# Kernel tuning notes

Measured on AMD Instinct MI355X. Metric: run time of the kernel, lower is better.

## Reference

```python
import jax, jax.numpy as jnp
import numpy as np

N = 4096
NFEAT = 512
NHID = 64
NHEADS = 8
NCLASS = 41
ALPHA = 0.2          # LeakyReLU negative slope
NEG = -9e15          # mask fill value from the torch code
EDGE_P = 0.004       # ~16 avg degree


def _xavier_uniform(key, shape, gain=1.414):
    fan_in, fan_out = shape[-2], shape[-1]
    limit = gain * np.sqrt(6.0 / (fan_in + fan_out))
    return jax.random.uniform(key, shape, jnp.float32, -limit, limit)


def setup_inputs() -> dict:
    key = jax.random.key(0)
    ks = jax.random.split(key, 6)
    x = jax.random.normal(ks[0], (N, NFEAT), jnp.float32)
    # sparse random graph, densified (module calls adj.to_dense()); add self-loops
    adj = (jax.random.uniform(ks[1], (N, N)) < EDGE_P).astype(jnp.float32)
    adj = jnp.maximum(adj, jnp.eye(N, dtype=jnp.float32))
    # 8 attention heads (nfeat -> nhid), stacked
    W_heads = _xavier_uniform(ks[2], (NHEADS, NFEAT, NHID))
    a_heads = _xavier_uniform(ks[3], (NHEADS, 2 * NHID, 1))
    # output attention layer (nhid*nheads -> nclass)
    W_out = _xavier_uniform(ks[4], (NHEADS * NHID, NCLASS))
    a_out = _xavier_uniform(ks[5], (2 * NCLASS, 1))
    return {"x": x, "adj": adj, "W_heads": W_heads, "a_heads": a_heads,
            "W_out": W_out, "a_out": a_out}


def _leaky_relu(e):
    return jnp.where(e > 0, e, ALPHA * e)


def reference(x, adj, W_heads, a_heads, W_out, a_out):
    # inference mode: all dropout layers are identity (training=False)
    mask = adj > 0                                   # [N, N]
    # ---- multi-head GAT layer (concat=True, ELU inside layer) ----
    Wh = jnp.einsum('nf,hfd->hnd', x, W_heads)       # [H, N, D]
    a1 = a_heads[:, :NHID, 0]                        # [H, D]
    a2 = a_heads[:, NHID:, 0]                        # [H, D]
    s1 = jnp.einsum('hnd,hd->hn', Wh, a1)            # [H, N]
    s2 = jnp.einsum('hnd,hd->hn', Wh, a2)            # [H, N]
    e = _leaky_relu(s1[:, :, None] + s2[:, None, :])  # [H, N, N]
    att = jax.nn.softmax(jnp.where(mask[None], e, NEG), axis=-1)
    h = jax.nn.elu(jnp.einsum('hnm,hmd->hnd', att, Wh))   # [H, N, D]
    h = jnp.transpose(h, (1, 0, 2)).reshape(N, NHEADS * NHID)  # concat heads
    # ---- output GAT layer (concat=False) + ELU (with_relu=True) ----
    Wh2 = h @ W_out                                  # [N, C]
    e2 = _leaky_relu(Wh2 @ a_out[:NCLASS] + (Wh2 @ a_out[NCLASS:]).T)  # [N, N]
    att2 = jax.nn.softmax(jnp.where(mask, e2, NEG), axis=-1)
    out = jax.nn.elu(att2 @ Wh2)                     # [N, C]
    # mode='t', multi_label falsy -> log_softmax
    return jax.nn.log_softmax(out, axis=1)
```

## Files before the change

### kernel.cpp

```cpp
#include <hip/hip_runtime.h>
#include <hip/hip_bf16.h>
#include <math.h>


#define N 4096
#define NFEAT 512
#define NHID 64
#define NHEADS 8
#define NCLASS 41
#define NCPAD 48
#define ALPHA 0.2f
#define ELLW 64

using short8  = __attribute__((ext_vector_type(8))) short;
using floatx4 = __attribute__((ext_vector_type(4))) float;

__device__ __forceinline__ float wred_max(float v) {
#pragma unroll
  for (int o = 32; o; o >>= 1) v = fmaxf(v, __shfl_xor(v, o, 64));
  return v;
}
__device__ __forceinline__ float wred_sum(float v) {
#pragma unroll
  for (int o = 32; o; o >>= 1) v += __shfl_xor(v, o, 64);
  return v;
}

__device__ __forceinline__ void split_bf16(float v, short& hi, short& lo) {
  __hip_bfloat16 hb = __float2bfloat16(v);
  float hf = __bfloat162float(hb);
  __hip_bfloat16 lb = __float2bfloat16(v - hf);
  hi = *reinterpret_cast<short*>(&hb);
  lo = *reinterpret_cast<short*>(&lb);
}

__global__ __launch_bounds__(256) void setup(const float* __restrict__ x,
                                             const float* __restrict__ W,
                                             const float* __restrict__ W_out,
                                             const float* __restrict__ adj,
                                             short* __restrict__ Xhi,
                                             short* __restrict__ Xlo,
                                             short* __restrict__ Wthi,
                                             short* __restrict__ Wtlo,
                                             short* __restrict__ WOhi,
                                             short* __restrict__ WOlo,
                                             int* __restrict__ cols,
                                             int* __restrict__ cnts) {
  if (blockIdx.x >= 3168) {
    __shared__ int c;
    const int row = blockIdx.x - 3168;
    if (threadIdx.x == 0) c = 0;
    __syncthreads();
    const float4* arow = (const float4*)(adj + (size_t)row * N);
    for (int j4 = threadIdx.x; j4 < N / 4; j4 += 256) {
      float4 v = arow[j4];
      if (v.x > 0.f) { int p = atomicAdd(&c, 1); if (p < ELLW) cols[row * ELLW + p] = j4 * 4 + 0; }
      if (v.y > 0.f) { int p = atomicAdd(&c, 1); if (p < ELLW) cols[row * ELLW + p] = j4 * 4 + 1; }
      if (v.z > 0.f) { int p = atomicAdd(&c, 1); if (p < ELLW) cols[row * ELLW + p] = j4 * 4 + 2; }
      if (v.w > 0.f) { int p = atomicAdd(&c, 1); if (p < ELLW) cols[row * ELLW + p] = j4 * 4 + 3; }
    }
    __syncthreads();
    if (threadIdx.x == 0) cnts[row] = min(c, ELLW);
  } else if (blockIdx.x < 2048) {
    const int t = blockIdx.x * 256 + threadIdx.x;
    const float4 v = ((const float4*)x)[t];
    short h0, l0, h1, l1, h2, l2, h3, l3;
    split_bf16(v.x, h0, l0);
    split_bf16(v.y, h1, l1);
    split_bf16(v.z, h2, l2);
    split_bf16(v.w, h3, l3);
    ((short4*)Xhi)[t] = make_short4(h0, h1, h2, h3);
    ((short4*)Xlo)[t] = make_short4(l0, l1, l2, l3);
  } else if (blockIdx.x < 3072) {
    const int t = (blockIdx.x - 2048) * 256 + threadIdx.x;
    const int h = t >> 15, r = t & 32767;
    const int d = r >> 9, k = r & 511;
    float v = W[(size_t)h * 32768 + (size_t)k * 64 + d];
    short hi, lo;
    split_bf16(v, hi, lo);
    Wthi[(size_t)h * 32768 + d * 512 + k] = hi;
    Wtlo[(size_t)h * 32768 + d * 512 + k] = lo;
  } else {
    const int t = (blockIdx.x - 3072) * 256 + threadIdx.x;
    const int c = t >> 9, k = t & 511;
    float v = (c < NCLASS) ? W_out[(size_t)k * NCLASS + c] : 0.f;
    short hi, lo;
    split_bf16(v, hi, lo);
    WOhi[c * 512 + k] = hi;
    WOlo[c * 512 + k] = lo;
  }
}

__global__ __launch_bounds__(256) void wh_gemm_mfma(
    const short* __restrict__ Xhi, const short* __restrict__ Xlo,
    const short* __restrict__ Wthi, const short* __restrict__ Wtlo,
    const float* __restrict__ a_heads,
    float* __restrict__ Wh, float* __restrict__ s1, float* __restrict__ s2) {
  __shared__ __align__(16) short Ahi[64 * 72];
  __shared__ __align__(16) short Alo[64 * 72];
  __shared__ __align__(16) short Bhi[64 * 72];
  __shared__ __align__(16) short Blo[64 * 72];
  const int id = blockIdx.x;
  const int h = (id >> 3) & 7;
  const int tile = (id & 7) + ((id >> 6) << 3);
  const int n0 = tile * 64;
  const int tid = threadIdx.x;
  const int w = tid >> 6, L = tid & 63;

  floatx4 acc[4];
#pragma unroll
  for (int f = 0; f < 4; f++) acc[f] = (floatx4){0.f, 0.f, 0.f, 0.f};

  for (int k0 = 0; k0 < NFEAT; k0 += 64) {
    __syncthreads();
#pragma unroll
    for (int i = 0; i < 2; i++) {
      const int g = tid + 256 * i;
      const int row = g >> 3, kg = (g & 7) * 8;
      const size_t asrc = (size_t)(n0 + row) * NFEAT + k0 + kg;
      *(uint4*)&Ahi[row * 72 + kg] = *(const uint4*)&Xhi[asrc];
      *(uint4*)&Alo[row * 72 + kg] = *(const uint4*)&Xlo[asrc];
      const size_t bsrc = (size_t)h * 32768 + (size_t)row * 512 + k0 + kg;
      *(uint4*)&Bhi[row * 72 + kg] = *(const uint4*)&Wthi[bsrc];
      *(uint4*)&Blo[row * 72 + kg] = *(const uint4*)&Wtlo[bsrc];
    }
    __syncthreads();
#pragma unroll
    for (int ks = 0; ks < 2; ks++) {
      const int koff = ks * 32 + (L >> 4) * 8;
      short8 ahi = *(const short8*)&Ahi[(w * 16 + (L & 15)) * 72 + koff];
      short8 alo = *(const short8*)&Alo[(w * 16 + (L & 15)) * 72 + koff];
#pragma unroll
      for (int f = 0; f < 4; f++) {
        short8 bhi = *(const short8*)&Bhi[(f * 16 + (L & 15)) * 72 + koff];
        short8 blo = *(const short8*)&Blo[(f * 16 + (L & 15)) * 72 + koff];
        acc[f] = __builtin_amdgcn_mfma_f32_16x16x32_bf16(ahi, bhi, acc[f], 0, 0, 0);
        acc[f] = __builtin_amdgcn_mfma_f32_16x16x32_bf16(ahi, blo, acc[f], 0, 0, 0);
        acc[f] = __builtin_amdgcn_mfma_f32_16x16x32_bf16(alo, bhi, acc[f], 0, 0, 0);
      }
    }
  }

  const int q = L >> 4, c16 = L & 15;
  float a1v[4], a2v[4];
#pragma unroll
  for (int f = 0; f < 4; f++) {
    a1v[f] = a_heads[h * 128 + f * 16 + c16];
    a2v[f] = a_heads[h * 128 + 64 + f * 16 + c16];
  }
  float p1[4] = {0.f, 0.f, 0.f, 0.f}, p2[4] = {0.f, 0.f, 0.f, 0.f};
#pragma unroll
  for (int f = 0; f < 4; f++)
#pragma unroll
    for (int r = 0; r < 4; r++) {
      const float vv = acc[f][r];
      const int row = n0 + w * 16 + q * 4 + r;
      Wh[((size_t)(h << 12) + row) * NHID + f * 16 + c16] = vv;
      p1[r] += vv * a1v[f];
      p2[r] += vv * a2v[f];
    }
#pragma unroll
  for (int r = 0; r < 4; r++)
#pragma unroll
    for (int o = 1; o < 16; o <<= 1) {
      p1[r] += __shfl_xor(p1[r], o, 64);
      p2[r] += __shfl_xor(p2[r], o, 64);
    }
  if (c16 == 0) {
    const int row = n0 + w * 16 + q * 4;
#pragma unroll
    for (int r = 0; r < 4; r++) {
      s1[(h << 12) + row + r] = p1[r];
      s2[(h << 12) + row + r] = p2[r];
    }
  }
}

__global__ __launch_bounds__(256) void att1_kernel(
    const float* __restrict__ Wh, const float* __restrict__ s1,
    const float* __restrict__ s2, const int* __restrict__ cols,
    const int* __restrict__ cnts, short* __restrict__ Hhi,
    short* __restrict__ Hlo) {
  __shared__ float pj[4][68];
  __shared__ int jj[4][68];
  const int w = threadIdx.x >> 6, lane = threadIdx.x & 63;
  const int pair = blockIdx.x * 4 + w;
  const int h = pair >> 12, i = pair & (N - 1);
  const int cnt = cnts[i];
  const float s1i = s1[(h << 12) + i];
  const float* s2h = s2 + (h << 12);
  float e0 = -1e30f;
  int j0 = 0;
  if (lane < cnt) {
    j0 = cols[i * ELLW + lane];
    float t = s1i + s2h[j0];
    e0 = t > 0.f ? t : ALPHA * t;
  }
  const float m = wred_max(e0);
  float p = (lane < cnt) ? expf(e0 - m) : 0.f;
  const float S = wred_sum(p);
  p *= 1.f / S;
  pj[w][lane] = p;
  jj[w][lane] = (lane < cnt) ? j0 : 0;
  if (lane < 4) { pj[w][64 + lane] = 0.f; jj[w][64 + lane] = 0; }
  __syncthreads();
  const int grp = lane >> 4, c4 = lane & 15;
  const float* Whh = Wh + (((size_t)h << 12)) * NHID;
  float4 acc = make_float4(0.f, 0.f, 0.f, 0.f);
  for (int t0 = 0; t0 < cnt; t0 += 4) {
    const float pt = pj[w][t0 + grp];
    const int jt = jj[w][t0 + grp];
    const float4 v = *(const float4*)&Whh[(size_t)jt * NHID + c4 * 4];
    acc.x += pt * v.x; acc.y += pt * v.y; acc.z += pt * v.z; acc.w += pt * v.w;
  }
#pragma unroll
  for (int off = 16; off <= 32; off <<= 1) {
    acc.x += __shfl_xor(acc.x, off, 64);
    acc.y += __shfl_xor(acc.y, off, 64);
    acc.z += __shfl_xor(acc.z, off, 64);
    acc.w += __shfl_xor(acc.w, off, 64);
  }
  if (grp == 0) {
    const float o0 = acc.x > 0.f ? acc.x : expf(acc.x) - 1.f;
    const float o1 = acc.y > 0.f ? acc.y : expf(acc.y) - 1.f;
    const float o2 = acc.z > 0.f ? acc.z : expf(acc.z) - 1.f;
    const float o3 = acc.w > 0.f ? acc.w : expf(acc.w) - 1.f;
    short h0, l0, h1, l1, h2, l2, h3, l3;
    split_bf16(o0, h0, l0);
    split_bf16(o1, h1, l1);
    split_bf16(o2, h2, l2);
    split_bf16(o3, h3, l3);
    const size_t base = (size_t)i * 512 + h * 64 + c4 * 4;
    *(short4*)&Hhi[base] = make_short4(h0, h1, h2, h3);
    *(short4*)&Hlo[base] = make_short4(l0, l1, l2, l3);
  }
}

__global__ __launch_bounds__(256) void gemm2_mfma(
    const short* __restrict__ Hhi, const short* __restrict__ Hlo,
    const short* __restrict__ WOhi, const short* __restrict__ WOlo,
    const float* __restrict__ a_out,
    float* __restrict__ Wh2, float* __restrict__ s1b, float* __restrict__ s2b) {
  __shared__ __align__(16) short Ahi[64 * 72];
  __shared__ __align__(16) short Alo[64 * 72];
  __shared__ __align__(16) short Bhi[NCPAD * 72];
  __shared__ __align__(16) short Blo[NCPAD * 72];
  const int n0 = blockIdx.x * 64;
  const int tid = threadIdx.x;
  const int w = tid >> 6, L = tid & 63;

  floatx4 acc[3];
#pragma unroll
  for (int f = 0; f < 3; f++) acc[f] = (floatx4){0.f, 0.f, 0.f, 0.f};

  for (int k0 = 0; k0 < 512; k0 += 64) {
    __syncthreads();
#pragma unroll
    for (int i = 0; i < 2; i++) {
      const int g = tid + 256 * i;
      const int row = g >> 3, kg = (g & 7) * 8;
      const size_t asrc = (size_t)(n0 + row) * 512 + k0 + kg;
      *(uint4*)&Ahi[row * 72 + kg] = *(const uint4*)&Hhi[asrc];
      *(uint4*)&Alo[row * 72 + kg] = *(const uint4*)&Hlo[asrc];
      if (g < NCPAD * 8) {
        const size_t bsrc = (size_t)row * 512 + k0 + kg;
        *(uint4*)&Bhi[row * 72 + kg] = *(const uint4*)&WOhi[bsrc];
        *(uint4*)&Blo[row * 72 + kg] = *(const uint4*)&WOlo[bsrc];
      }
    }
    __syncthreads();
#pragma unroll
    for (int ks = 0; ks < 2; ks++) {
      const int koff = ks * 32 + (L >> 4) * 8;
      short8 ahi = *(const short8*)&Ahi[(w * 16 + (L & 15)) * 72 + koff];
      short8 alo = *(const short8*)&Alo[(w * 16 + (L & 15)) * 72 + koff];
#pragma unroll
      for (int f = 0; f < 3; f++) {
        short8 bhi = *(const short8*)&Bhi[(f * 16 + (L & 15)) * 72 + koff];
        short8 blo = *(const short8*)&Blo[(f * 16 + (L & 15)) * 72 + koff];
        acc[f] = __builtin_amdgcn_mfma_f32_16x16x32_bf16(ahi, bhi, acc[f], 0, 0, 0);
        acc[f] = __builtin_amdgcn_mfma_f32_16x16x32_bf16(ahi, blo, acc[f], 0, 0, 0);
        acc[f] = __builtin_amdgcn_mfma_f32_16x16x32_bf16(alo, bhi, acc[f], 0, 0, 0);
      }
    }
  }

  const int q = L >> 4, c16 = L & 15;
  float a1v[3], a2v[3];
#pragma unroll
  for (int f = 0; f < 3; f++) {
    const int col = f * 16 + c16;
    a1v[f] = (col < NCLASS) ? a_out[col] : 0.f;
    a2v[f] = (col < NCLASS) ? a_out[NCLASS + col] : 0.f;
  }
  float p1[4] = {0.f, 0.f, 0.f, 0.f}, p2[4] = {0.f, 0.f, 0.f, 0.f};
#pragma unroll
  for (int f = 0; f < 3; f++)
#pragma unroll
    for (int r = 0; r < 4; r++) {
      const float vv = acc[f][r];
      const int col = f * 16 + c16;
      const int row = n0 + w * 16 + q * 4 + r;
      if (col < NCLASS) Wh2[(size_t)row * NCLASS + col] = vv;
      p1[r] += vv * a1v[f];
      p2[r] += vv * a2v[f];
    }
#pragma unroll
  for (int r = 0; r < 4; r++)
#pragma unroll
    for (int o = 1; o < 16; o <<= 1) {
      p1[r] += __shfl_xor(p1[r], o, 64);
      p2[r] += __shfl_xor(p2[r], o, 64);
    }
  if (c16 == 0) {
    const int row = n0 + w * 16 + q * 4;
#pragma unroll
    for (int r = 0; r < 4; r++) {
      s1b[row + r] = p1[r];
      s2b[row + r] = p2[r];
    }
  }
}

__global__ __launch_bounds__(256) void att2_kernel(const float* __restrict__ Wh2,
                                                   const float* __restrict__ s1b,
                                                   const float* __restrict__ s2b,
                                                   const int* __restrict__ cols,
                                                   const int* __restrict__ cnts,
                                                   float* __restrict__ out) {
  __shared__ float pj[4][64];
  __shared__ int jj[4][64];
  const int w = threadIdx.x >> 6, lane = threadIdx.x & 63;
  const int i = blockIdx.x * 4 + w;
  const int cnt = cnts[i];
  const float s1i = s1b[i];
  float e0 = -1e30f;
  int j0 = 0;
  if (lane < cnt) {
    j0 = cols[i * ELLW + lane];
    float t = s1i + s2b[j0];
    e0 = t > 0.f ? t : ALPHA * t;
  }
  const float m = wred_max(e0);
  float p = (lane < cnt) ? expf(e0 - m) : 0.f;
  const float S = wred_sum(p);
  p *= 1.f / S;
  pj[w][lane] = p;
  jj[w][lane] = (lane < cnt) ? j0 : 0;
  __syncthreads();
  float acc = 0.f;
  for (int t = 0; t < cnt; t++) {
    const float pt = pj[w][t];
    const int jt = jj[w][t];
    if (lane < NCLASS) acc += pt * Wh2[(size_t)jt * NCLASS + lane];
  }
  const float o = acc > 0.f ? acc : expf(acc) - 1.f;
  const float vv = (lane < NCLASS) ? o : -1e30f;
  const float mm = wred_max(vv);
  const float ex = (lane < NCLASS) ? expf(o - mm) : 0.f;
  const float SS = wred_sum(ex);
  if (lane < NCLASS) out[(size_t)i * NCLASS + lane] = o - mm - logf(SS);
}

extern "C" void kernel_launch(void* const* d_in, const int* in_sizes, int n_in,
                              void* d_out, int out_size, void* d_ws, size_t ws_size,
                              hipStream_t stream) {
  const float* x       = (const float*)d_in[0];
  const float* adj     = (const float*)d_in[1];
  const float* W_heads = (const float*)d_in[2];
  const float* a_heads = (const float*)d_in[3];
  const float* W_out   = (const float*)d_in[4];
  const float* a_out   = (const float*)d_in[5];
  float* out = (float*)d_out;

  float* ws   = (float*)d_ws;
  float* Wh   = ws;
  float* s1   = Wh + (size_t)NHEADS * N * NHID;
  float* s2   = s1 + NHEADS * N;
  float* Wh2  = s2 + NHEADS * N;
  float* s1b  = Wh2 + (size_t)N * NCLASS;
  float* s2b  = s1b + N;
  int* cnts   = (int*)(s2b + N);
  int* cols   = cnts + N;
  short* Xhi  = (short*)(cols + N * ELLW);
  short* Xlo  = Xhi + (size_t)N * NFEAT;
  short* Wthi = Xlo + (size_t)N * NFEAT;
  short* Wtlo = Wthi + (size_t)NHEADS * NHID * NFEAT;
  short* WOhi = Wtlo + (size_t)NHEADS * NHID * NFEAT;
  short* WOlo = WOhi + (size_t)NCPAD * 512;
  short* Hhi  = WOlo + (size_t)NCPAD * 512;
  short* Hlo  = Hhi + (size_t)N * NFEAT;

  hipLaunchKernelGGL(setup, dim3(7264), dim3(256), 0, stream,
                     x, W_heads, W_out, adj, Xhi, Xlo, Wthi, Wtlo, WOhi, WOlo, cols, cnts);
  hipLaunchKernelGGL(wh_gemm_mfma, dim3(NHEADS * N / 64), dim3(256), 0, stream,
                     Xhi, Xlo, Wthi, Wtlo, a_heads, Wh, s1, s2);
  hipLaunchKernelGGL(att1_kernel, dim3(NHEADS * N / 4), dim3(256), 0, stream,
                     Wh, s1, s2, cols, cnts, Hhi, Hlo);
  hipLaunchKernelGGL(gemm2_mfma, dim3(N / 64), dim3(256), 0, stream,
                     Hhi, Hlo, WOhi, WOlo, a_out, Wh2, s1b, s2b);
  hipLaunchKernelGGL(att2_kernel, dim3(N / 4), dim3(256), 0, stream,
                     Wh2, s1b, s2b, cols, cnts, out);
}
```

Measured before the change: 169.1 us.

## Tile W transpose via LDS, 2x row tiles in wh_gemm, split-K gemm2

The setup W transpose now reads 64x64 tiles with coalesced float4 loads, transposes them through shared memory and writes short8 vectors, replacing scattered per-element accesses. wh_gemm_mfma drops to 128 threads, with each wave computing two 16-row tiles so every B fragment is reused twice. gemm2 becomes a split-K kernel over 16-row blocks: four waves each take a quarter of K straight from global memory and are reduced through LDS. This gives gemm2 four times as many blocks and removes its LDS staging, at the cost of a shared-memory reduction step and fewer waves per block in wh_gemm.

```diff
diff --git a/kernel.cpp b/kernel.cpp
--- a/kernel.cpp
+++ b/kernel.cpp
@@ -46,9 +46,9 @@
                                              short* __restrict__ WOlo,
                                              int* __restrict__ cols,
                                              int* __restrict__ cnts) {
-  if (blockIdx.x >= 3168) {
+  if (blockIdx.x >= 2208) {
     __shared__ int c;
-    const int row = blockIdx.x - 3168;
+    const int row = blockIdx.x - 2208;
     if (threadIdx.x == 0) c = 0;
     __syncthreads();
     const float4* arow = (const float4*)(adj + (size_t)row * N);
@@ -71,17 +71,40 @@
     split_bf16(v.w, h3, l3);
     ((short4*)Xhi)[t] = make_short4(h0, h1, h2, h3);
     ((short4*)Xlo)[t] = make_short4(l0, l1, l2, l3);
-  } else if (blockIdx.x < 3072) {
-    const int t = (blockIdx.x - 2048) * 256 + threadIdx.x;
-    const int h = t >> 15, r = t & 32767;
-    const int d = r >> 9, k = r & 511;
-    float v = W[(size_t)h * 32768 + (size_t)k * 64 + d];
-    short hi, lo;
-    split_bf16(v, hi, lo);
-    Wthi[(size_t)h * 32768 + d * 512 + k] = hi;
-    Wtlo[(size_t)h * 32768 + d * 512 + k] = lo;
+  } else if (blockIdx.x < 2112) {
+    __shared__ float tile[64][65];
+    const int idx = blockIdx.x - 2048;
+    const int h = idx >> 3, k0 = (idx & 7) * 64;
+    const int t = threadIdx.x;
+#pragma unroll
+    for (int i = 0; i < 4; i++) {
+      const int g = t + 256 * i;
+      const int r = g >> 4, c4 = g & 15;
+      const float4 v = *(const float4*)&W[(size_t)h * 32768 + (size_t)(k0 + r) * 64 + c4 * 4];
+      tile[r][c4 * 4 + 0] = v.x;
+      tile[r][c4 * 4 + 1] = v.y;
+      tile[r][c4 * 4 + 2] = v.z;
+      tile[r][c4 * 4 + 3] = v.w;
+    }
+    __syncthreads();
+#pragma unroll
+    for (int i = 0; i < 2; i++) {
+      const int g = t + 256 * i;
+      const int d = g >> 3, kg = (g & 7) * 8;
+      short8 hv, lv;
+#pragma unroll
+      for (int j = 0; j < 8; j++) {
+        short hh, ll;
+        split_bf16(tile[kg + j][d], hh, ll);
+        hv[j] = hh;
+        lv[j] = ll;
+      }
+      const size_t dst = (size_t)h * 32768 + (size_t)d * 512 + k0 + kg;
+      *(short8*)&Wthi[dst] = hv;
+      *(short8*)&Wtlo[dst] = lv;
+    }
   } else {
-    const int t = (blockIdx.x - 3072) * 256 + threadIdx.x;
+    const int t = (blockIdx.x - 2112) * 256 + threadIdx.x;
     const int c = t >> 9, k = t & 511;
     float v = (c < NCLASS) ? W_out[(size_t)k * NCLASS + c] : 0.f;
     short hi, lo;
@@ -91,7 +114,7 @@
   }
 }
 
-__global__ __launch_bounds__(256) void wh_gemm_mfma(
+__global__ __launch_bounds__(128) void wh_gemm_mfma(
     const short* __restrict__ Xhi, const short* __restrict__ Xlo,
     const short* __restrict__ Wthi, const short* __restrict__ Wtlo,
     const float* __restrict__ a_heads,
@@ -107,15 +130,17 @@
   const int tid = threadIdx.x;
   const int w = tid >> 6, L = tid & 63;
 
-  floatx4 acc[4];
-#pragma unroll
-  for (int f = 0; f < 4; f++) acc[f] = (floatx4){0.f, 0.f, 0.f, 0.f};
+  floatx4 acc[2][4];
+#pragma unroll
+  for (int rt = 0; rt < 2; rt++)
+#pragma unroll
+    for (int f = 0; f < 4; f++) acc[rt][f] = (floatx4){0.f, 0.f, 0.f, 0.f};
 
   for (int k0 = 0; k0 < NFEAT; k0 += 64) {
     __syncthreads();
 #pragma unroll
-    for (int i = 0; i < 2; i++) {
-      const int g = tid + 256 * i;
+    for (int i = 0; i < 4; i++) {
+      const int g = tid + 128 * i;
       const int row = g >> 3, kg = (g & 7) * 8;
       const size_t asrc = (size_t)(n0 + row) * NFEAT + k0 + kg;
       *(uint4*)&Ahi[row * 72 + kg] = *(const uint4*)&Xhi[asrc];
@@ -128,15 +153,21 @@
 #pragma unroll
     for (int ks = 0; ks < 2; ks++) {
       const int koff = ks * 32 + (L >> 4) * 8;
-      short8 ahi = *(const short8*)&Ahi[(w * 16 + (L & 15)) * 72 + koff];
-      short8 alo = *(const short8*)&Alo[(w * 16 + (L & 15)) * 72 + koff];
+      const int abase = (w * 32 + (L & 15)) * 72 + koff;
+      short8 ahi0 = *(const short8*)&Ahi[abase];
+      short8 alo0 = *(const short8*)&Alo[abase];
+      short8 ahi1 = *(const short8*)&Ahi[abase + 16 * 72];
+      short8 alo1 = *(const short8*)&Alo[abase + 16 * 72];
 #pragma unroll
       for (int f = 0; f < 4; f++) {
         short8 bhi = *(const short8*)&Bhi[(f * 16 + (L & 15)) * 72 + koff];
         short8 blo = *(const short8*)&Blo[(f * 16 + (L & 15)) * 72 + koff];
-        acc[f] = __builtin_amdgcn_mfma_f32_16x16x32_bf16(ahi, bhi, acc[f], 0, 0, 0);
-        acc[f] = __builtin_amdgcn_mfma_f32_16x16x32_bf16(ahi, blo, acc[f], 0, 0, 0);
-        acc[f] = __builtin_amdgcn_mfma_f32_16x16x32_bf16(alo, bhi, acc[f], 0, 0, 0);
+        acc[0][f] = __builtin_amdgcn_mfma_f32_16x16x32_bf16(ahi0, bhi, acc[0][f], 0, 0, 0);
+        acc[0][f] = __builtin_amdgcn_mfma_f32_16x16x32_bf16(ahi0, blo, acc[0][f], 0, 0, 0);
+        acc[0][f] = __builtin_amdgcn_mfma_f32_16x16x32_bf16(alo0, bhi, acc[0][f], 0, 0, 0);
+        acc[1][f] = __builtin_amdgcn_mfma_f32_16x16x32_bf16(ahi1, bhi, acc[1][f], 0, 0, 0);
+        acc[1][f] = __builtin_amdgcn_mfma_f32_16x16x32_bf16(ahi1, blo, acc[1][f], 0, 0, 0);
+        acc[1][f] = __builtin_amdgcn_mfma_f32_16x16x32_bf16(alo1, bhi, acc[1][f], 0, 0, 0);
       }
     }
   }
@@ -148,30 +179,33 @@
     a1v[f] = a_heads[h * 128 + f * 16 + c16];
     a2v[f] = a_heads[h * 128 + 64 + f * 16 + c16];
   }
-  float p1[4] = {0.f, 0.f, 0.f, 0.f}, p2[4] = {0.f, 0.f, 0.f, 0.f};
-#pragma unroll
-  for (int f = 0; f < 4; f++)
-#pragma unroll
-    for (int r = 0; r < 4; r++) {
-      const float vv = acc[f][r];
-      const int row = n0 + w * 16 + q * 4 + r;
-      Wh[((size_t)(h << 12) + row) * NHID + f * 16 + c16] = vv;
-      p1[r] += vv * a1v[f];
-      p2[r] += vv * a2v[f];
-    }
-#pragma unroll
-  for (int r = 0; r < 4; r++)
-#pragma unroll
-    for (int o = 1; o < 16; o <<= 1) {
-      p1[r] += __shfl_xor(p1[r], o, 64);
-      p2[r] += __shfl_xor(p2[r], o, 64);
-    }
-  if (c16 == 0) {
-    const int row = n0 + w * 16 + q * 4;
-#pragma unroll
-    for (int r = 0; r < 4; r++) {
-      s1[(h << 12) + row + r] = p1[r];
-      s2[(h << 12) + row + r] = p2[r];
+#pragma unroll
+  for (int rt = 0; rt < 2; rt++) {
+    float p1[4] = {0.f, 0.f, 0.f, 0.f}, p2[4] = {0.f, 0.f, 0.f, 0.f};
+#pragma unroll
+    for (int f = 0; f < 4; f++)
+#pragma unroll
+      for (int r = 0; r < 4; r++) {
+        const float vv = acc[rt][f][r];
+        const int row = n0 + w * 32 + rt * 16 + q * 4 + r;
+        Wh[((size_t)(h << 12) + row) * NHID + f * 16 + c16] = vv;
+        p1[r] += vv * a1v[f];
+        p2[r] += vv * a2v[f];
+      }
+#pragma unroll
+    for (int r = 0; r < 4; r++)
+#pragma unroll
+      for (int o = 1; o < 16; o <<= 1) {
+        p1[r] += __shfl_xor(p1[r], o, 64);
+        p2[r] += __shfl_xor(p2[r], o, 64);
+      }
+    if (c16 == 0) {
+      const int row = n0 + w * 32 + rt * 16 + q * 4;
+#pragma unroll
+      for (int r = 0; r < 4; r++) {
+        s1[(h << 12) + row + r] = p1[r];
+        s2[(h << 12) + row + r] = p2[r];
+      }
     }
   }
 }
@@ -241,83 +275,74 @@
     const short* __restrict__ WOhi, const short* __restrict__ WOlo,
     const float* __restrict__ a_out,
     float* __restrict__ Wh2, float* __restrict__ s1b, float* __restrict__ s2b) {
-  __shared__ __align__(16) short Ahi[64 * 72];
-  __shared__ __align__(16) short Alo[64 * 72];
-  __shared__ __align__(16) short Bhi[NCPAD * 72];
-  __shared__ __align__(16) short Blo[NCPAD * 72];
-  const int n0 = blockIdx.x * 64;
+  __shared__ float red[3][64][12];
+  const int n0 = blockIdx.x * 16;
   const int tid = threadIdx.x;
   const int w = tid >> 6, L = tid & 63;
+  const int r15 = L & 15;
 
   floatx4 acc[3];
 #pragma unroll
   for (int f = 0; f < 3; f++) acc[f] = (floatx4){0.f, 0.f, 0.f, 0.f};
 
-  for (int k0 = 0; k0 < 512; k0 += 64) {
-    __syncthreads();
-#pragma unroll
-    for (int i = 0; i < 2; i++) {
-      const int g = tid + 256 * i;
-      const int row = g >> 3, kg = (g & 7) * 8;
-      const size_t asrc = (size_t)(n0 + row) * 512 + k0 + kg;
-      *(uint4*)&Ahi[row * 72 + kg] = *(const uint4*)&Hhi[asrc];
-      *(uint4*)&Alo[row * 72 + kg] = *(const uint4*)&Hlo[asrc];
-      if (g < NCPAD * 8) {
-        const size_t bsrc = (size_t)row * 512 + k0 + kg;
-        *(uint4*)&Bhi[row * 72 + kg] = *(const uint4*)&WOhi[bsrc];
-        *(uint4*)&Blo[row * 72 + kg] = *(const uint4*)&WOlo[bsrc];
-      }
-    }
-    __syncthreads();
-#pragma unroll
-    for (int ks = 0; ks < 2; ks++) {
-      const int koff = ks * 32 + (L >> 4) * 8;
-      short8 ahi = *(const short8*)&Ahi[(w * 16 + (L & 15)) * 72 + koff];
-      short8 alo = *(const short8*)&Alo[(w * 16 + (L & 15)) * 72 + koff];
-#pragma unroll
-      for (int f = 0; f < 3; f++) {
-        short8 bhi = *(const short8*)&Bhi[(f * 16 + (L & 15)) * 72 + koff];
-        short8 blo = *(const short8*)&Blo[(f * 16 + (L & 15)) * 72 + koff];
-        acc[f] = __builtin_amdgcn_mfma_f32_16x16x32_bf16(ahi, bhi, acc[f], 0, 0, 0);
-        acc[f] = __builtin_amdgcn_mfma_f32_16x16x32_bf16(ahi, blo, acc[f], 0, 0, 0);
-        acc[f] = __builtin_amdgcn_mfma_f32_16x16x32_bf16(alo, bhi, acc[f], 0, 0, 0);
-      }
-    }
-  }
-
-  const int q = L >> 4, c16 = L & 15;
-  float a1v[3], a2v[3];
-#pragma unroll
-  for (int f = 0; f < 3; f++) {
-    const int col = f * 16 + c16;
-    a1v[f] = (col < NCLASS) ? a_out[col] : 0.f;
-    a2v[f] = (col < NCLASS) ? a_out[NCLASS + col] : 0.f;
-  }
-  float p1[4] = {0.f, 0.f, 0.f, 0.f}, p2[4] = {0.f, 0.f, 0.f, 0.f};
-#pragma unroll
-  for (int f = 0; f < 3; f++)
-#pragma unroll
-    for (int r = 0; r < 4; r++) {
-      const float vv = acc[f][r];
+#pragma unroll
+  for (int ks = 0; ks < 4; ks++) {
+    const int koff = w * 128 + ks * 32 + (L >> 4) * 8;
+    const short8 ahi = *(const short8*)&Hhi[(size_t)(n0 + r15) * 512 + koff];
+    const short8 alo = *(const short8*)&Hlo[(size_t)(n0 + r15) * 512 + koff];
+#pragma unroll
+    for (int f = 0; f < 3; f++) {
+      const short8 bhi = *(const short8*)&WOhi[(size_t)(f * 16 + r15) * 512 + koff];
+      const short8 blo = *(const short8*)&WOlo[(size_t)(f * 16 + r15) * 512 + koff];
+      acc[f] = __builtin_amdgcn_mfma_f32_16x16x32_bf16(ahi, bhi, acc[f], 0, 0, 0);
+      acc[f] = __builtin_amdgcn_mfma_f32_16x16x32_bf16(ahi, blo, acc[f], 0, 0, 0);
+      acc[f] = __builtin_amdgcn_mfma_f32_16x16x32_bf16(alo, bhi, acc[f], 0, 0, 0);
+    }
+  }
+
+  if (w) {
+#pragma unroll
+    for (int f = 0; f < 3; f++)
+#pragma unroll
+      for (int r = 0; r < 4; r++) red[w - 1][L][f * 4 + r] = acc[f][r];
+  }
+  __syncthreads();
+  if (w == 0) {
+    const int q = L >> 4, c16 = r15;
+    float a1v[3], a2v[3];
+#pragma unroll
+    for (int f = 0; f < 3; f++) {
       const int col = f * 16 + c16;
-      const int row = n0 + w * 16 + q * 4 + r;
-      if (col < NCLASS) Wh2[(size_t)row * NCLASS + col] = vv;
-      p1[r] += vv * a1v[f];
-      p2[r] += vv * a2v[f];
-    }
-#pragma unroll
-  for (int r = 0; r < 4; r++)
-#pragma unroll
-    for (int o = 1; o < 16; o <<= 1) {
-      p1[r] += __shfl_xor(p1[r], o, 64);
-      p2[r] += __shfl_xor(p2[r], o, 64);
-    }
-  if (c16 == 0) {
-    const int row = n0 + w * 16 + q * 4;
-#pragma unroll
-    for (int r = 0; r < 4; r++) {
-      s1b[row + r] = p1[r];
-      s2b[row + r] = p2[r];
+      a1v[f] = (col < NCLASS) ? a_out[col] : 0.f;
+      a2v[f] = (col < NCLASS) ? a_out[NCLASS + col] : 0.f;
+    }
+    float p1[4] = {0.f, 0.f, 0.f, 0.f}, p2[4] = {0.f, 0.f, 0.f, 0.f};
+#pragma unroll
+    for (int f = 0; f < 3; f++)
+#pragma unroll
+      for (int r = 0; r < 4; r++) {
+        const float vv = acc[f][r] + red[0][L][f * 4 + r] + red[1][L][f * 4 + r] +
+                         red[2][L][f * 4 + r];
+        const int col = f * 16 + c16;
+        const int row = n0 + q * 4 + r;
+        if (col < NCLASS) Wh2[(size_t)row * NCLASS + col] = vv;
+        p1[r] += vv * a1v[f];
+        p2[r] += vv * a2v[f];
+      }
+#pragma unroll
+    for (int r = 0; r < 4; r++)
+#pragma unroll
+      for (int o = 1; o < 16; o <<= 1) {
+        p1[r] += __shfl_xor(p1[r], o, 64);
+        p2[r] += __shfl_xor(p2[r], o, 64);
+      }
+    if (c16 == 0) {
+      const int row = n0 + q * 4;
+#pragma unroll
+      for (int r = 0; r < 4; r++) {
+        s1b[row + r] = p1[r];
+        s2b[row + r] = p2[r];
+      }
     }
   }
 }
@@ -391,13 +416,13 @@
   short* Hhi  = WOlo + (size_t)NCPAD * 512;
   short* Hlo  = Hhi + (size_t)N * NFEAT;
 
-  hipLaunchKernelGGL(setup, dim3(7264), dim3(256), 0, stream,
+  hipLaunchKernelGGL(setup, dim3(6304), dim3(256), 0, stream,
                      x, W_heads, W_out, adj, Xhi, Xlo, Wthi, Wtlo, WOhi, WOlo, cols, cnts);
-  hipLaunchKernelGGL(wh_gemm_mfma, dim3(NHEADS * N / 64), dim3(256), 0, stream,
+  hipLaunchKernelGGL(wh_gemm_mfma, dim3(NHEADS * N / 64), dim3(128), 0, stream,
                      Xhi, Xlo, Wthi, Wtlo, a_heads, Wh, s1, s2);
   hipLaunchKernelGGL(att1_kernel, dim3(NHEADS * N / 4), dim3(256), 0, stream,
                      Wh, s1, s2, cols, cnts, Hhi, Hlo);
-  hipLaunchKernelGGL(gemm2_mfma, dim3(N / 64), dim3(256), 0, stream,
+  hipLaunchKernelGGL(gemm2_mfma, dim3(N / 16), dim3(256), 0, stream,
                      Hhi, Hlo, WOhi, WOlo, a_out, Wh2, s1b, s2b);
   hipLaunchKernelGGL(att2_kernel, dim3(N / 4), dim3(256), 0, stream,
                      Wh2, s1b, s2b, cols, cnts, out);
```

New measurement: 159.6 us. 1.06x faster.
